# Kernel tuning notes

Hardware: AMD Instinct MI355X
Metric: run time of the kernel (lower is better)

The kernel has to match this reference:

```python
import jax, jax.numpy as jnp
import numpy as np

B, T, DIM = 8, 1024, 512
H, DK, L = 8, 64, 32          # heads, dim_key, rel_pos_length
DH = H * DK                    # dim_hidden = 512
DOUT = 512
EPS = 1e-5


def setup_inputs() -> dict:
    key = jax.random.key(0)
    ks = jax.random.split(key, 5)
    x = jax.random.normal(ks[0], (B, T, DIM), jnp.float32)
    Wqkv = jax.random.normal(ks[1], (3 * DH, DIM), jnp.float32) * (1.0 / np.sqrt(DIM))
    Wout = jax.random.normal(ks[2], (DOUT, DH), jnp.float32) * (1.0 / np.sqrt(DH))
    bout = jax.random.normal(ks[3], (DOUT,), jnp.float32) * 0.01
    rel_positions = jax.random.normal(ks[4], (2 * L - 1, DK), jnp.float32)
    bn_gamma = jnp.ones((DK,), jnp.float32)
    bn_beta = jnp.zeros((DK,), jnp.float32)
    return {"x": x, "Wqkv": Wqkv, "Wout": Wout, "bout": bout,
            "rel_positions": rel_positions, "bn_gamma": bn_gamma, "bn_beta": bn_beta}


def reference(x, Wqkv, Wout, bout, rel_positions, bn_gamma, bn_beta):
    b, t, f = x.shape
    # Conv1d(dim, 3*dim_hidden, 1, bias=False) on x.transpose(1,2) == pointwise matmul
    qkv = jnp.einsum('btf,of->bot', x, Wqkv)          # (b, 3*DH, t)
    q, k, v = jnp.split(qkv, 3, axis=1)
    q = q.reshape(b * H, DK, t)
    k = k.reshape(b * H, DK, t)
    v = v.reshape(b * H, DK, t)

    # linear-attention core: softmax over sequence for k, tiny DKxDK context
    k = jax.nn.softmax(k, axis=-1)
    context = jnp.einsum('ndt,net->nde', k, v)        # (n, DK, DK)
    content_out = jnp.einsum('nde,ndt->net', context, q)  # (n, DK, t); norm_queries=False

    # Relative-position path. Original builds one-hot It (t,t,2L-1) and
    # Pt = einsum('tir,rd->tid', It, rel_positions); then
    # St = einsum('ndt,tid->nit', q, Pt); rel = einsum('nit,net->net', St, v)
    #     = v * (sum_i St)[:,None,:].
    # sum_i Pt[t,i,d] = sum over valid band offsets of rel_positions -> band matmul.
    r = jnp.arange(-(L - 1), L)                       # (2L-1,)
    pos = jnp.arange(t)
    tgt = pos[:, None] + r[None, :]                   # i = x + r
    valid = ((tgt >= 0) & (tgt < t)).astype(x.dtype)  # (t, 2L-1)
    Psum = valid @ rel_positions                      # (t, DK) == Pt.sum(axis=1)
    S = jnp.einsum('ndt,td->nt', q, Psum)             # (n, t)
    rel = v * S[:, None, :]                           # (n, DK, t)

    # BatchNorm1d(DK), training-mode batch stats over (n, t), biased variance
    mu = jnp.mean(rel, axis=(0, 2), keepdims=True)
    var = jnp.mean((rel - mu) ** 2, axis=(0, 2), keepdims=True)
    rel = (rel - mu) * jax.lax.rsqrt(var + EPS) * bn_gamma[None, :, None] + bn_beta[None, :, None]

    out = (content_out + rel).reshape(b, DH, t)
    # Conv1d(dim_hidden, dim_out, 1) with bias
    return jnp.einsum('od,bdt->bot', Wout, out) + bout[None, :, None]
```

## Files before the change

### kernel.cpp

```cpp
#include <hip/hip_runtime.h>
#include <hip/hip_bf16.h>


typedef short bf16x8 __attribute__((ext_vector_type(8)));
typedef float f32x4 __attribute__((ext_vector_type(4)));

static __device__ __forceinline__ unsigned short f2bf(float f) {
  __hip_bfloat16 h = __float2bfloat16(f);
  return *reinterpret_cast<unsigned short*>(&h);
}
static __device__ __forceinline__ float bf2f(unsigned short u) {
  union { unsigned int i; float f; } c; c.i = ((unsigned int)u) << 16;
  return c.f;
}
static __device__ __forceinline__ void gl_lds16(const unsigned short* g, unsigned short* l) {
  __builtin_amdgcn_global_load_lds((const __attribute__((address_space(1))) unsigned int*)g,
                                   (__attribute__((address_space(3))) unsigned int*)l,
                                   16, 0, 0);
}

__global__ __launch_bounds__(256) void prep(const float* __restrict__ x,
                                            const float* __restrict__ wqkv,
                                            const float* __restrict__ wout,
                                            const float* __restrict__ relpos,
                                            unsigned short* __restrict__ xb,
                                            unsigned short* __restrict__ wqkvb,
                                            unsigned short* __restrict__ woutb,
                                            float* __restrict__ PsumT) {
  const int bx = blockIdx.x;
  if (bx < 5120) {
    int j = bx * 256 + threadIdx.x;
    const float* src; unsigned short* dst;
    if (j < 1048576) { src = x; dst = xb; }
    else if (j < 1245184) { j -= 1048576; src = wqkv; dst = wqkvb; }
    else { j -= 1245184; src = wout; dst = woutb; }
    float4 v = ((const float4*)src)[j];
    ushort4 o = {f2bf(v.x), f2bf(v.y), f2bf(v.z), f2bf(v.w)};
    ((ushort4*)dst)[j] = o;
  } else {
    const int idx = bx - 5120;
    const int d = idx >> 2;
    const int t = (idx & 3) * 256 + threadIdx.x;
    float acc = 0.f;
    for (int j = 0; j < 63; ++j) {
      int i = t + j - 31;
      float v = relpos[j * 64 + d];
      if (i >= 0 && i < 1024) acc += v;
    }
    PsumT[d * 1024 + t] = acc;
  }
}


__global__ __launch_bounds__(256) void gemm_qkv(const unsigned short* __restrict__ A,
                                                const unsigned short* __restrict__ B,
                                                unsigned short* __restrict__ C) {
  __shared__ alignas(16) unsigned short As[8192];
  __shared__ alignas(16) unsigned short Bs[8192];
  const int tid = threadIdx.x;
  const int wave = tid >> 6, lane = tid & 63;
  const int bm = blockIdx.y * 128, bn = blockIdx.x * 128;
  const int wm = (wave >> 1) * 64, wn = (wave & 1) * 64;
  const int fr = lane & 15, cq = lane >> 4;
  const unsigned short* srcA[4];
  const unsigned short* srcB[4];
#pragma unroll
  for (int j = 0; j < 4; ++j) {
    const int s = tid + j * 256;
    const int row = s >> 3, cp = s & 7;
    const int c = cp ^ (row & 7);
    srcA[j] = A + (size_t)(bm + row) * 512 + c * 8;
    srcB[j] = B + (size_t)(bn + row) * 512 + c * 8;
  }
  int offA[4][2], offB[4][2];
#pragma unroll
  for (int i = 0; i < 4; ++i)
#pragma unroll
    for (int ks = 0; ks < 2; ++ks) {
      int ra = wm + i * 16 + fr;
      offA[i][ks] = (ra * 8 + ((ks * 4 + cq) ^ (ra & 7))) * 8;
      int rb = wn + i * 16 + fr;
      offB[i][ks] = (rb * 8 + ((ks * 4 + cq) ^ (rb & 7))) * 8;
    }
  f32x4 acc[4][4];
#pragma unroll
  for (int i = 0; i < 4; ++i)
#pragma unroll
    for (int j = 0; j < 4; ++j) acc[i][j] = (f32x4){0.f, 0.f, 0.f, 0.f};
  for (int k0 = 0; k0 < 512; k0 += 64) {
    __syncthreads();
#pragma unroll
    for (int j = 0; j < 4; ++j) {
      gl_lds16(srcA[j] + k0, As + (wave * 64 + j * 256) * 8);
      gl_lds16(srcB[j] + k0, Bs + (wave * 64 + j * 256) * 8);
    }
    __builtin_amdgcn_s_waitcnt(0);
    __syncthreads();
#pragma unroll
    for (int ks = 0; ks < 2; ++ks) {
      bf16x8 af[4], bq[4];
#pragma unroll
      for (int mi = 0; mi < 4; ++mi) af[mi] = *(const bf16x8*)(As + offA[mi][ks]);
#pragma unroll
      for (int nj = 0; nj < 4; ++nj) bq[nj] = *(const bf16x8*)(Bs + offB[nj][ks]);
#pragma unroll
      for (int mi = 0; mi < 4; ++mi)
#pragma unroll
        for (int nj = 0; nj < 4; ++nj)
          acc[mi][nj] = __builtin_amdgcn_mfma_f32_16x16x32_bf16(af[mi], bq[nj], acc[mi][nj], 0, 0, 0);
    }
  }
#pragma unroll
  for (int mi = 0; mi < 4; ++mi) {
    const int row0 = bm + wm + mi * 16 + (lane >> 4) * 4;
#pragma unroll
    for (int nj = 0; nj < 4; ++nj) {
      const int col = bn + wn + nj * 16 + fr;
#pragma unroll
      for (int rr = 0; rr < 4; ++rr)
        C[(size_t)(row0 + rr) * 8192 + col] = f2bf(acc[mi][nj][rr]);
    }
  }
}

__global__ __launch_bounds__(256) void gemm_out(const unsigned short* __restrict__ A,
                                                const unsigned short* __restrict__ B,
                                                const float* __restrict__ bias,
                                                float* __restrict__ out) {
  __shared__ alignas(16) unsigned short As[8192];
  __shared__ alignas(16) unsigned short Bs[8192];
  const int tid = threadIdx.x;
  const int wave = tid >> 6, lane = tid & 63;
  const int bm = blockIdx.y * 128, bn = blockIdx.x * 128;
  const int wm = (wave >> 1) * 64, wn = (wave & 1) * 64;
  const int fr = lane & 15, cq = lane >> 4;
  const unsigned short* srcA[4];
  const unsigned short* srcB[4];
#pragma unroll
  for (int j = 0; j < 4; ++j) {
    const int s = tid + j * 256;
    const int row = s >> 3, cp = s & 7;
    const int c = cp ^ (row & 7);
    srcA[j] = A + (size_t)(bm + row) * 512 + c * 8;
    srcB[j] = B + (size_t)(bn + row) * 512 + c * 8;
  }
  int offA[4][2], offB[4][2];
#pragma unroll
  for (int i = 0; i < 4; ++i)
#pragma unroll
    for (int ks = 0; ks < 2; ++ks) {
      int ra = wm + i * 16 + fr;
      offA[i][ks] = (ra * 8 + ((ks * 4 + cq) ^ (ra & 7))) * 8;
      int rb = wn + i * 16 + fr;
      offB[i][ks] = (rb * 8 + ((ks * 4 + cq) ^ (rb & 7))) * 8;
    }
  f32x4 acc[4][4];
#pragma unroll
  for (int i = 0; i < 4; ++i)
#pragma unroll
    for (int j = 0; j < 4; ++j) acc[i][j] = (f32x4){0.f, 0.f, 0.f, 0.f};
  for (int k0 = 0; k0 < 512; k0 += 64) {
    __syncthreads();
#pragma unroll
    for (int j = 0; j < 4; ++j) {
      gl_lds16(srcA[j] + k0, As + (wave * 64 + j * 256) * 8);
      gl_lds16(srcB[j] + k0, Bs + (wave * 64 + j * 256) * 8);
    }
    __builtin_amdgcn_s_waitcnt(0);
    __syncthreads();
#pragma unroll
    for (int ks = 0; ks < 2; ++ks) {
      bf16x8 af[4], bq[4];
#pragma unroll
      for (int mi = 0; mi < 4; ++mi) af[mi] = *(const bf16x8*)(As + offA[mi][ks]);
#pragma unroll
      for (int nj = 0; nj < 4; ++nj) bq[nj] = *(const bf16x8*)(Bs + offB[nj][ks]);
#pragma unroll
      for (int mi = 0; mi < 4; ++mi)
#pragma unroll
        for (int nj = 0; nj < 4; ++nj)
          acc[mi][nj] = __builtin_amdgcn_mfma_f32_16x16x32_bf16(af[mi], bq[nj], acc[mi][nj], 0, 0, 0);
    }
  }
#pragma unroll
  for (int mi = 0; mi < 4; ++mi) {
    const int row0 = bm + wm + mi * 16 + (lane >> 4) * 4;
#pragma unroll
    for (int nj = 0; nj < 4; ++nj) {
      const int col = bn + wn + nj * 16 + fr;
      const int b = col >> 10, t = col & 1023;
#pragma unroll
      for (int rr = 0; rr < 4; ++rr)
        out[(size_t)b * 524288 + (size_t)(row0 + rr) * 1024 + t] = acc[mi][nj][rr] + bias[row0 + rr];
    }
  }
}

__global__ __launch_bounds__(256) void stats(const unsigned short* __restrict__ qkv,
                                             const float* __restrict__ PsumT,
                                             float* __restrict__ S,
                                             float* __restrict__ part1,
                                             float* __restrict__ part2,
                                             float* __restrict__ lse) {
  const int bx = blockIdx.x;
  const int tid = threadIdx.x, wave = tid >> 6, lane = tid & 63;
  __shared__ float swave[4][64];
  __shared__ float s_lds[64];
  if (bx < 1024) {
    const int tc = bx & 15, n = bx >> 4;
    const int b = n >> 3, h = n & 7;
    const int t0 = tc * 64;
    const int tg = lane & 7, rg = lane >> 3;
    const unsigned short* qbase = qkv + (size_t)(h * 64) * 8192 + b * 1024 + t0 + tg * 8;
    const float* pbase = PsumT + t0 + tg * 8;
    float acc[8] = {0.f};
#pragma unroll
    for (int i = 0; i < 2; ++i) {
      const int d = wave * 16 + i * 8 + rg;
      bf16x8 qv = *(const bf16x8*)(qbase + (size_t)d * 8192);
      float4 p0 = *(const float4*)(pbase + d * 1024);
      float4 p1 = *(const float4*)(pbase + d * 1024 + 4);
      float p[8] = {p0.x, p0.y, p0.z, p0.w, p1.x, p1.y, p1.z, p1.w};
#pragma unroll
      for (int j = 0; j < 8; ++j) acc[j] = fmaf(bf2f((unsigned short)qv[j]), p[j], acc[j]);
    }
#pragma unroll
    for (int off = 8; off < 64; off <<= 1)
#pragma unroll
      for (int j = 0; j < 8; ++j) acc[j] += __shfl_xor(acc[j], off);
    if (rg == 0) {
#pragma unroll
      for (int j = 0; j < 8; ++j) swave[wave][tg * 8 + j] = acc[j];
    }
    __syncthreads();
    if (tid < 64) {
      float s = swave[0][tid] + swave[1][tid] + swave[2][tid] + swave[3][tid];
      s_lds[tid] = s;
      S[(size_t)n * 1024 + t0 + tid] = s;
    }
    __syncthreads();
    const unsigned short* vbase = qkv + (size_t)(1024 + h * 64) * 8192 + b * 1024 + t0 + tg * 8;
    const int blk = n * 16 + tc;
    float sv[8];
#pragma unroll
    for (int j = 0; j < 8; ++j) sv[j] = s_lds[tg * 8 + j];
#pragma unroll
    for (int i = 0; i < 2; ++i) {
      const int e = wave * 16 + i * 8 + rg;
      bf16x8 vv = *(const bf16x8*)(vbase + (size_t)e * 8192);
      float a1 = 0.f, a2 = 0.f;
#pragma unroll
      for (int j = 0; j < 8; ++j) {
        float val = bf2f((unsigned short)vv[j]) * sv[j];
        a1 += val;
        a2 = fmaf(val, val, a2);
      }
#pragma unroll
      for (int off = 1; off < 8; off <<= 1) {
        a1 += __shfl_xor(a1, off);
        a2 += __shfl_xor(a2, off);
      }
      if (tg == 0) {
        part1[e * 1024 + blk] = a1;
        part2[e * 1024 + blk] = a2;
      }
    }
  } else {
    const int r = (bx - 1024) * 4 + wave;
    const int hd = r >> 3, b = r & 7;
    const unsigned short* row = qkv + (size_t)(512 + hd) * 8192 + b * 1024 + lane * 16;
    uint4 u0 = *(const uint4*)row;
    uint4 u1 = *(const uint4*)(row + 8);
    const unsigned short* us0 = (const unsigned short*)&u0;
    const unsigned short* us1 = (const unsigned short*)&u1;
    float f[16];
#pragma unroll
    for (int i = 0; i < 8; ++i) { f[i] = bf2f(us0[i]); f[8 + i] = bf2f(us1[i]); }
    float m = f[0];
#pragma unroll
    for (int i = 1; i < 16; ++i) m = fmaxf(m, f[i]);
#pragma unroll
    for (int off = 32; off; off >>= 1) m = fmaxf(m, __shfl_xor(m, off));
    float s = 0.f;
#pragma unroll
    for (int i = 0; i < 16; ++i) s += __expf(f[i] - m);
#pragma unroll
    for (int off = 32; off; off >>= 1) s += __shfl_xor(s, off);
    if (lane == 0) lse[r] = m + __logf(s);
  }
}

__global__ __launch_bounds__(256) void context_mfma(const unsigned short* __restrict__ qkv,
                                                    const float* __restrict__ lse,
                                                    float* __restrict__ ctx_part) {
  const int tc = blockIdx.x, n = blockIdx.y;
  const int b = n >> 3, h = n & 7;
  const int tid = threadIdx.x;
  const int wave = tid >> 6, lane = tid & 63;
  __shared__ float ls[64];
  __shared__ float ctx_l[64][68];
  if (tid < 64) ls[tid] = lse[(h * 64 + tid) * 8 + b];
  __syncthreads();
  const int fr = lane & 15, fk = (lane >> 4) * 8;
  const size_t colbase = (size_t)b * 1024 + tc * 256 + wave * 64;
  const unsigned short* kbase = qkv + (size_t)(512 + h * 64) * 8192 + colbase;
  const unsigned short* vbase = qkv + (size_t)(1024 + h * 64) * 8192 + colbase;
  f32x4 acc[4][4];
#pragma unroll
  for (int i = 0; i < 4; ++i)
#pragma unroll
    for (int j = 0; j < 4; ++j) acc[i][j] = (f32x4){0.f, 0.f, 0.f, 0.f};
#pragma unroll
  for (int ks = 0; ks < 2; ++ks) {
    const int tb = ks * 32 + fk;
    bf16x8 aF[4], bF[4];
#pragma unroll
    for (int dt = 0; dt < 4; ++dt) {
      const int row = dt * 16 + fr;
      bf16x8 kv = *(const bf16x8*)(kbase + (size_t)row * 8192 + tb);
      const float lv = ls[row];
      bf16x8 pv;
#pragma unroll
      for (int j = 0; j < 8; ++j)
        pv[j] = (short)f2bf(__expf(bf2f((unsigned short)kv[j]) - lv));
      aF[dt] = pv;
    }
#pragma unroll
    for (int et = 0; et < 4; ++et)
      bF[et] = *(const bf16x8*)(vbase + (size_t)(et * 16 + fr) * 8192 + tb);
#pragma unroll
    for (int dt = 0; dt < 4; ++dt)
#pragma unroll
      for (int et = 0; et < 4; ++et)
        acc[dt][et] = __builtin_amdgcn_mfma_f32_16x16x32_bf16(aF[dt], bF[et], acc[dt][et], 0, 0, 0);
  }
#pragma unroll
  for (int w = 0; w < 4; ++w) {
    if (wave == w) {
#pragma unroll
      for (int dt = 0; dt < 4; ++dt)
#pragma unroll
        for (int et = 0; et < 4; ++et) {
          const int col = et * 16 + fr;
#pragma unroll
          for (int rr = 0; rr < 4; ++rr) {
            const int rw = dt * 16 + (lane >> 4) * 4 + rr;
            if (w == 0) ctx_l[rw][col] = acc[dt][et][rr];
            else ctx_l[rw][col] += acc[dt][et][rr];
          }
        }
    }
    __syncthreads();
  }
  float* outp = ctx_part + ((size_t)tc * 64 + n) * 4096;
  for (int i = tid * 4; i < 4096; i += 1024) {
    const int rw = i >> 6, cc = i & 63;
    *(float4*)(outp + i) = *(const float4*)&ctx_l[rw][cc];
  }
}

__global__ __launch_bounds__(256) void reduce2(const float* __restrict__ part,
                                               float* __restrict__ ctx,
                                               const float* __restrict__ part1,
                                               const float* __restrict__ part2,
                                               const float* __restrict__ gamma,
                                               const float* __restrict__ beta,
                                               float* __restrict__ scale,
                                               float* __restrict__ shift) {
  const int bx = blockIdx.x;
  const int tid = threadIdx.x;
  if (bx < 256) {
    const int i4 = bx * 256 + tid;
    const float4* p = (const float4*)part;
    float4 a = p[i4], b = p[65536 + i4], c = p[131072 + i4], d = p[196608 + i4];
    float4 s = {a.x + b.x + c.x + d.x, a.y + b.y + c.y + d.y,
                a.z + b.z + c.z + d.z, a.w + b.w + c.w + d.w};
    ((float4*)ctx)[i4] = s;
  } else {
    const int e = bx - 256;
    float a1 = 0.f, a2 = 0.f;
#pragma unroll
    for (int i = 0; i < 4; ++i) {
      a1 += part1[e * 1024 + i * 256 + tid];
      a2 += part2[e * 1024 + i * 256 + tid];
    }
#pragma unroll
    for (int off = 32; off; off >>= 1) {
      a1 += __shfl_down(a1, off);
      a2 += __shfl_down(a2, off);
    }
    __shared__ float r1[4], r2[4];
    const int w = tid >> 6, lane = tid & 63;
    if (lane == 0) { r1[w] = a1; r2[w] = a2; }
    __syncthreads();
    if (tid == 0) {
      float s1 = r1[0] + r1[1] + r1[2] + r1[3];
      float s2 = r2[0] + r2[1] + r2[2] + r2[3];
      const float cnt = 65536.0f;
      float mu = s1 / cnt;
      float var = s2 / cnt - mu * mu;
      float sc = gamma[e] * rsqrtf(var + 1e-5f);
      scale[e] = sc;
      shift[e] = beta[e] - mu * sc;
    }
  }
}

__global__ __launch_bounds__(256) void content_out_t(const unsigned short* __restrict__ qkv,
                                                     const float* __restrict__ ctx,
                                                     const float* __restrict__ S,
                                                     const float* __restrict__ scale,
                                                     const float* __restrict__ shift,
                                                     unsigned short* __restrict__ outT) {
  const int chunk = blockIdx.x, n = blockIdx.y;
  const int b = n >> 3, h = n & 7;
  const int t0 = chunk * 64;
  __shared__ float cs[4096];
  __shared__ alignas(16) unsigned short T[64][72];
  const float* cp = ctx + (size_t)n * 4096;
  for (int i = threadIdx.x * 4; i < 4096; i += 1024)
    *(float4*)&cs[i] = *(const float4*)&cp[i];
  __syncthreads();
  const int tid = threadIdx.x;
  const int e0 = (tid & 15) * 4;
  const int tq = (tid >> 4) * 4;
  const unsigned short* qbase = qkv + (size_t)(h * 64) * 8192 + b * 1024 + t0 + tq;
  float acc[4][4] = {{0.f}};
  for (int d = 0; d < 64; ++d) {
    float4 cv = *(const float4*)&cs[d * 64 + e0];
    ushort4 qu = *(const ushort4*)(qbase + (size_t)d * 8192);
    float qa[4] = {bf2f(qu.x), bf2f(qu.y), bf2f(qu.z), bf2f(qu.w)};
    float ca[4] = {cv.x, cv.y, cv.z, cv.w};
#pragma unroll
    for (int a = 0; a < 4; ++a)
#pragma unroll
      for (int c = 0; c < 4; ++c)
        acc[a][c] = fmaf(ca[a], qa[c], acc[a][c]);
  }
  float4 svv = *(const float4*)(S + (size_t)n * 1024 + t0 + tq);
  float sa[4] = {svv.x, svv.y, svv.z, svv.w};
  float4 scv = *(const float4*)(scale + e0);
  float4 shv = *(const float4*)(shift + e0);
  float sc[4] = {scv.x, scv.y, scv.z, scv.w};
  float sh[4] = {shv.x, shv.y, shv.z, shv.w};
#pragma unroll
  for (int a = 0; a < 4; ++a) {
    ushort4 vu = *(const ushort4*)(qkv + (size_t)(1024 + h * 64 + e0 + a) * 8192 + b * 1024 + t0 + tq);
    float va[4] = {bf2f(vu.x), bf2f(vu.y), bf2f(vu.z), bf2f(vu.w)};
#pragma unroll
    for (int c = 0; c < 4; ++c)
      T[tq + c][e0 + a] = f2bf(fmaf(va[c] * sa[c], sc[a], acc[a][c] + sh[a]));
  }
  __syncthreads();
  const int tl = tid >> 2, dq = (tid & 3) * 16;
  uint4 r0 = *(uint4*)&T[tl][dq];
  uint4 r1 = *(uint4*)&T[tl][dq + 8];
  unsigned short* op = outT + ((size_t)(b * 1024 + t0 + tl)) * 512 + h * 64 + dq;
  *(uint4*)op = r0;
  *(uint4*)(op + 8) = r1;
}

extern "C" void kernel_launch(void* const* d_in, const int* in_sizes, int n_in,
                              void* d_out, int out_size, void* d_ws, size_t ws_size,
                              hipStream_t stream) {
  const float* x       = (const float*)d_in[0];
  const float* Wqkv    = (const float*)d_in[1];
  const float* Wout    = (const float*)d_in[2];
  const float* bout    = (const float*)d_in[3];
  const float* relpos  = (const float*)d_in[4];
  const float* gamma   = (const float*)d_in[5];
  const float* beta    = (const float*)d_in[6];
  float* out = (float*)d_out;

  float* ws = (float*)d_ws;
  unsigned short* qkvb  = (unsigned short*)ws;
  float* p = ws + 6291456;
  unsigned short* xb    = (unsigned short*)p;  p += 2097152;
  unsigned short* wqkvb = (unsigned short*)p;  p += 393216;
  unsigned short* woutb = (unsigned short*)p;  p += 131072;
  float* ctx_part = p;  p += 1048576;
  float* ctx      = p;  p += 262144;
  float* PsumT    = p;  p += 65536;
  float* S        = p;  p += 65536;
  float* lse      = p;  p += 4096;
  float* part1    = p;  p += 65536;
  float* part2    = p;  p += 65536;
  float* scale    = p;  p += 64;
  float* shift    = p;  p += 64;
  unsigned short* outT = (unsigned short*)p;

  prep<<<5376, 256, 0, stream>>>(x, Wqkv, Wout, relpos, xb, wqkvb, woutb, PsumT);
  gemm_qkv<<<dim3(64, 12), 256, 0, stream>>>(wqkvb, xb, qkvb);
  stats<<<2048, 256, 0, stream>>>(qkvb, PsumT, S, part1, part2, lse);
  context_mfma<<<dim3(4, 64), 256, 0, stream>>>(qkvb, lse, ctx_part);
  reduce2<<<320, 256, 0, stream>>>(ctx_part, ctx, part1, part2, gamma, beta, scale, shift);
  content_out_t<<<dim3(16, 64), 256, 0, stream>>>(qkvb, ctx, S, scale, shift, outT);
  gemm_out<<<dim3(64, 4), 256, 0, stream>>>(woutb, outT, bout, out);
}
```

Before: 164.5 us.

## Double-buffer LDS tiles in the QKV and output GEMMs

Both bf16 MFMA GEMMs now use two LDS buffers per operand. The next K-slice is loaded asynchronously with global_load_lds while the current slice is computed, and there is one barrier per iteration instead of two. The explicit full waitcnt is removed, so visibility of the new tile relies on the waits emitted at __syncthreads. This doubles LDS per block to 64 KB, which may reduce the number of blocks resident per CU.

```diff
diff --git a/kernel.cpp b/kernel.cpp
--- a/kernel.cpp
+++ b/kernel.cpp
@@ -55,8 +55,8 @@
 __global__ __launch_bounds__(256) void gemm_qkv(const unsigned short* __restrict__ A,
                                                 const unsigned short* __restrict__ B,
                                                 unsigned short* __restrict__ C) {
-  __shared__ alignas(16) unsigned short As[8192];
-  __shared__ alignas(16) unsigned short Bs[8192];
+  __shared__ alignas(16) unsigned short As[2][8192];
+  __shared__ alignas(16) unsigned short Bs[2][8192];
   const int tid = threadIdx.x;
   const int wave = tid >> 6, lane = tid & 63;
   const int bm = blockIdx.y * 128, bn = blockIdx.x * 128;
@@ -87,29 +87,40 @@
   for (int i = 0; i < 4; ++i)
 #pragma unroll
     for (int j = 0; j < 4; ++j) acc[i][j] = (f32x4){0.f, 0.f, 0.f, 0.f};
-  for (int k0 = 0; k0 < 512; k0 += 64) {
-    __syncthreads();
+
+  auto stage = [&](int sel, int k0) {
 #pragma unroll
     for (int j = 0; j < 4; ++j) {
-      gl_lds16(srcA[j] + k0, As + (wave * 64 + j * 256) * 8);
-      gl_lds16(srcB[j] + k0, Bs + (wave * 64 + j * 256) * 8);
-    }
-    __builtin_amdgcn_s_waitcnt(0);
-    __syncthreads();
+      gl_lds16(srcA[j] + k0, &As[sel][(wave * 64 + j * 256) * 8]);
+      gl_lds16(srcB[j] + k0, &Bs[sel][(wave * 64 + j * 256) * 8]);
+    }
+  };
+  auto compute = [&](int sel) {
 #pragma unroll
     for (int ks = 0; ks < 2; ++ks) {
       bf16x8 af[4], bq[4];
 #pragma unroll
-      for (int mi = 0; mi < 4; ++mi) af[mi] = *(const bf16x8*)(As + offA[mi][ks]);
-#pragma unroll
-      for (int nj = 0; nj < 4; ++nj) bq[nj] = *(const bf16x8*)(Bs + offB[nj][ks]);
+      for (int mi = 0; mi < 4; ++mi) af[mi] = *(const bf16x8*)&As[sel][offA[mi][ks]];
+#pragma unroll
+      for (int nj = 0; nj < 4; ++nj) bq[nj] = *(const bf16x8*)&Bs[sel][offB[nj][ks]];
 #pragma unroll
       for (int mi = 0; mi < 4; ++mi)
 #pragma unroll
         for (int nj = 0; nj < 4; ++nj)
           acc[mi][nj] = __builtin_amdgcn_mfma_f32_16x16x32_bf16(af[mi], bq[nj], acc[mi][nj], 0, 0, 0);
     }
-  }
+  };
+
+  stage(0, 0);
+  __syncthreads();
+#pragma unroll
+  for (int t = 0; t < 7; ++t) {
+    stage((t + 1) & 1, (t + 1) * 64);
+    compute(t & 1);
+    __syncthreads();
+  }
+  compute(1);
+
 #pragma unroll
   for (int mi = 0; mi < 4; ++mi) {
     const int row0 = bm + wm + mi * 16 + (lane >> 4) * 4;
@@ -127,8 +138,8 @@
                                                 const unsigned short* __restrict__ B,
                                                 const float* __restrict__ bias,
                                                 float* __restrict__ out) {
-  __shared__ alignas(16) unsigned short As[8192];
-  __shared__ alignas(16) unsigned short Bs[8192];
+  __shared__ alignas(16) unsigned short As[2][8192];
+  __shared__ alignas(16) unsigned short Bs[2][8192];
   const int tid = threadIdx.x;
   const int wave = tid >> 6, lane = tid & 63;
   const int bm = blockIdx.y * 128, bn = blockIdx.x * 128;
@@ -159,29 +170,40 @@
   for (int i = 0; i < 4; ++i)
 #pragma unroll
     for (int j = 0; j < 4; ++j) acc[i][j] = (f32x4){0.f, 0.f, 0.f, 0.f};
-  for (int k0 = 0; k0 < 512; k0 += 64) {
-    __syncthreads();
+
+  auto stage = [&](int sel, int k0) {
 #pragma unroll
     for (int j = 0; j < 4; ++j) {
-      gl_lds16(srcA[j] + k0, As + (wave * 64 + j * 256) * 8);
-      gl_lds16(srcB[j] + k0, Bs + (wave * 64 + j * 256) * 8);
-    }
-    __builtin_amdgcn_s_waitcnt(0);
-    __syncthreads();
+      gl_lds16(srcA[j] + k0, &As[sel][(wave * 64 + j * 256) * 8]);
+      gl_lds16(srcB[j] + k0, &Bs[sel][(wave * 64 + j * 256) * 8]);
+    }
+  };
+  auto compute = [&](int sel) {
 #pragma unroll
     for (int ks = 0; ks < 2; ++ks) {
       bf16x8 af[4], bq[4];
 #pragma unroll
-      for (int mi = 0; mi < 4; ++mi) af[mi] = *(const bf16x8*)(As + offA[mi][ks]);
-#pragma unroll
-      for (int nj = 0; nj < 4; ++nj) bq[nj] = *(const bf16x8*)(Bs + offB[nj][ks]);
+      for (int mi = 0; mi < 4; ++mi) af[mi] = *(const bf16x8*)&As[sel][offA[mi][ks]];
+#pragma unroll
+      for (int nj = 0; nj < 4; ++nj) bq[nj] = *(const bf16x8*)&Bs[sel][offB[nj][ks]];
 #pragma unroll
       for (int mi = 0; mi < 4; ++mi)
 #pragma unroll
         for (int nj = 0; nj < 4; ++nj)
           acc[mi][nj] = __builtin_amdgcn_mfma_f32_16x16x32_bf16(af[mi], bq[nj], acc[mi][nj], 0, 0, 0);
     }
-  }
+  };
+
+  stage(0, 0);
+  __syncthreads();
+#pragma unroll
+  for (int t = 0; t < 7; ++t) {
+    stage((t + 1) & 1, (t + 1) * 64);
+    compute(t & 1);
+    __syncthreads();
+  }
+  compute(1);
+
 #pragma unroll
   for (int mi = 0; mi < 4; ++mi) {
     const int row0 = bm + wm + mi * 16 + (lane >> 4) * 4;
```

Measured after the change: 157.9 us. -4.0%, faster.
